# Kernel tuning notes

Measured on AMD Instinct MI355X. Metric: run time of the kernel, lower is better.

The kernel has to match this reference:

```python
import jax, jax.numpy as jnp
import numpy as np

WEIGHT = 1e-7
SIGMA_RGB = 15.0
SCALE = 0.5


def _nearest_resize(x, oh, ow):
    # PyTorch F.interpolate mode='nearest': src_idx = floor(dst * in/out)
    n, c, h, w = x.shape
    yi = (jnp.arange(oh) * (h / oh)).astype(jnp.int32)
    xi = (jnp.arange(ow) * (w / ow)).astype(jnp.int32)
    return x[:, :, yi][:, :, :, xi]


def _bilinear_resize(x, oh, ow):
    # PyTorch bilinear, align_corners=False: src = max((i+0.5)*in/out - 0.5, 0)
    n, k, h, w = x.shape

    def idx(o, s):
        src = jnp.maximum((jnp.arange(o, dtype=jnp.float32) + 0.5) * (s / o) - 0.5, 0.0)
        lo = jnp.floor(src).astype(jnp.int32)
        hi = jnp.minimum(lo + 1, s - 1)
        return lo, hi, src - lo

    ylo, yhi, fy = idx(oh, h)
    xlo, xhi, fx = idx(ow, w)
    top = x[:, :, ylo][:, :, :, xlo] * (1.0 - fx) + x[:, :, ylo][:, :, :, xhi] * fx
    bot = x[:, :, yhi][:, :, :, xlo] * (1.0 - fx) + x[:, :, yhi][:, :, :, xhi] * fx
    return top * (1.0 - fy)[:, None] + bot * fy[:, None]


def _bilateral_AS(feat, seg):
    # feat: [P,3] color features / sigma_rgb; seg: [K,P]
    # exact Gaussian color bilateral filter (what the permutohedral lattice approximates)
    sq = jnp.sum(feat * feat, axis=-1)                      # [P]
    d2 = sq[:, None] + sq[None, :] - 2.0 * (feat @ feat.T)  # [P,P]
    Kmat = jnp.exp(-0.5 * jnp.maximum(d2, 0.0))             # [P,P], symmetric
    return seg @ Kmat                                        # [K,P]


def setup_inputs() -> dict:
    key = jax.random.key(0)
    k1, k2 = jax.random.split(key)
    images = jax.random.uniform(k1, (4, 3, 128, 128), dtype=jnp.float32) * 255.0
    logits = jax.random.normal(k2, (4, 21, 128, 128), dtype=jnp.float32)
    segmentations = jax.nn.softmax(logits, axis=1)
    return {"images": images, "segmentations": segmentations}


def reference(images, segmentations):
    n, c, h, w = images.shape
    oh, ow = int(h * SCALE), int(w * SCALE)
    simg = _nearest_resize(images, oh, ow)            # [N,3,oh,ow]
    sseg = _bilinear_resize(segmentations, oh, ow)    # [N,K,oh,ow]
    P = oh * ow
    feats = simg.reshape(n, c, P).transpose(0, 2, 1) / SIGMA_RGB  # [N,P,3]
    segs = sseg.reshape(n, sseg.shape[1], P)                      # [N,K,P]
    AS = jax.vmap(_bilateral_AS)(feats, segs)                     # [N,K,P]
    loss = -jnp.sum(segs * AS) / jnp.float32(n)
    return (WEIGHT * loss).reshape(1)
```

## Files before the change

### kernel.cpp

```cpp
#include <hip/hip_runtime.h>


#define N_BATCH 4
#define IH 128
#define IW 128
#define P 4096
#define KC 21

using short8  = __attribute__((ext_vector_type(8))) short;
using floatx4 = __attribute__((ext_vector_type(4))) float;

static constexpr float INV_SIGMA = 1.0f / 15.0f;
static constexpr float LOG2E     = 1.4426950408889634f;
static constexpr float OUT_SCALE = -1e-7f / 4.0f;

#define ZP_OFF   0
#define ARGA_OFF 64
#define ARGB_OFF (ARGA_OFF + N_BATCH * P * 32)
#define SEG_OFF  (ARGB_OFF + N_BATCH * P * 32)

#define NFEAT (N_BATCH * P)
#define NSEG2 (N_BATCH * KC * P / 2)

__device__ __forceinline__ ushort f2bf(float x) {
    unsigned u = __builtin_bit_cast(unsigned, x);
    unsigned r = (u + 0x7FFFu + ((u >> 16) & 1u)) >> 16;
    return (ushort)r;
}
__device__ __forceinline__ float bf2f(ushort h) {
    return __builtin_bit_cast(float, (unsigned)h << 16);
}

__global__ void crf_prep(const float* __restrict__ img,
                         const float* __restrict__ seg,
                         char* __restrict__ wsb,
                         float* __restrict__ out)
{
    int t = blockIdx.x * blockDim.x + threadIdx.x;
    if (t < NFEAT) {
        if (t == 0) out[0] = 0.0f;
        if (t < 16) ((float*)(wsb + ZP_OFF))[t] = 0.0f;

        int n = t >> 12;
        int p = t & (P - 1);
        int y = p >> 6, x = p & 63;

        const float* ib = img + (size_t)n * 3 * IH * IW + (size_t)(2 * y) * IW + 2 * x;
        float f0 = ib[0] * INV_SIGMA;
        float f1 = ib[IH * IW] * INV_SIGMA;
        float f2 = ib[2 * IH * IW] * INV_SIGMA;
        float h = 0.5f * (f0 * f0 + f1 * f1 + f2 * f2);

        float fa0 = f0 * LOG2E, fa1 = f1 * LOG2E, fa2 = f2 * LOG2E;
        ushort ah0 = f2bf(fa0), ah1 = f2bf(fa1), ah2 = f2bf(fa2);
        ushort al0 = f2bf(fa0 - bf2f(ah0));
        ushort al1 = f2bf(fa1 - bf2f(ah1));
        ushort al2 = f2bf(fa2 - bf2f(ah2));
        float nhL = -h * LOG2E;
        ushort nhh = f2bf(nhL), nhl = f2bf(nhL - bf2f(nhh));
        ushort bh0 = f2bf(f0), bh1 = f2bf(f1), bh2 = f2bf(f2);
        ushort bl0 = f2bf(f0 - bf2f(bh0));
        ushort bl1 = f2bf(f1 - bf2f(bh1));
        ushort bl2 = f2bf(f2 - bf2f(bh2));
        float hL = h * LOG2E;
        ushort hbh = f2bf(hL), hbl = f2bf(hL - bf2f(hbh));

        const ushort ONE = 0x3F80, NEG1 = 0xBF80;
        ushort rA[16] = {ah0, ah1, ah2, ah0, ah1, ah2, al0, al1, al2, al0, al1, al2,
                         nhh, nhl, NEG1, NEG1};
        ushort rB[16] = {bh0, bh1, bh2, bl0, bl1, bl2, bh0, bh1, bh2, bl0, bl1, bl2,
                         ONE, ONE, hbh, hbl};

        short8 vA0, vA1, vB0, vB1;
#pragma unroll
        for (int j = 0; j < 8; ++j) {
            vA0[j] = (short)rA[j];     vA1[j] = (short)rA[8 + j];
            vB0[j] = (short)rB[j];     vB1[j] = (short)rB[8 + j];
        }
        short8* dA = (short8*)(wsb + ARGA_OFF + (size_t)t * 32);
        dA[0] = vA0; dA[1] = vA1;
        short8* dB = (short8*)(wsb + ARGB_OFF + (size_t)t * 32);
        dB[0] = vB0; dB[1] = vB1;

        char* sp = wsb + SEG_OFF + (size_t)t * 48;
        *(ushort*)(sp + 42) = 0;
        *(uint*)(sp + 44) = 0;
    } else if (t < NFEAT + NSEG2) {
        int u = t - NFEAT;
        int pp = (u & 2047) * 2;
        int nk = u >> 11;
        int n = nk / 21;
        int k = nk - n * 21;
        int y = pp >> 6, x0 = pp & 63;

        const float* r0 = seg + (size_t)nk * IH * IW + (size_t)(2 * y) * IW + 2 * x0;
        float4 a = *(const float4*)r0;
        float4 b = *(const float4*)(r0 + IW);
        float v0 = 0.25f * ((a.x + a.y) + (b.x + b.y));
        float v1 = 0.25f * ((a.z + a.w) + (b.z + b.w));
        char* d = wsb + SEG_OFF + (size_t)(n * P + pp) * 48 + k * 2;
        *(ushort*)d = f2bf(v0);
        *(ushort*)(d + 48) = f2bf(v1);
    }
}

__global__ __launch_bounds__(256, 4) void crf_pair(const char* __restrict__ wsb,
                                                   float* __restrict__ out)
{
    int n = blockIdx.z;
    int bp = blockIdx.y;
    int wave = threadIdx.x >> 6;
    int lane = threadIdx.x & 63;
    int quad = lane >> 4;
    int l16  = lane & 15;
    int w    = blockIdx.x * 4 + wave;

    const char* argA = wsb + ARGA_OFF + (size_t)n * P * 32;
    const char* argB = wsb + ARGB_OFF + (size_t)n * P * 32;
    const char* segT = wsb + SEG_OFF  + (size_t)n * P * 48;
    const char* zp   = wsb + ZP_OFF;

    int maskA = (quad < 2) ? ~0 : 0;
    int maskS = (quad < 3) ? ~0 : 0;
    const char* baseA_arg = (quad < 2) ? argA + quad * 16 : zp;
    const char* baseB_arg = (quad < 2) ? argB + quad * 16 : zp;
    const char* base_seg  = (quad < 3) ? segT + quad * 16 : zp;
    const int dA = 16384 & maskA;
    const int dS = 24576 & maskS;

    int s0 = 4 * bp;
    int s1 = 4 * (63 - bp);

    short8 aA0[4], aS0[4], aA1[4], aS1[4];
#pragma unroll
    for (int ii = 0; ii < 4; ++ii) {
        int r0 = (s0 + ii) * 16 + l16;
        int r1 = (s1 + ii) * 16 + l16;
        aA0[ii] = *(const short8*)(baseA_arg + ((r0 << 5) & maskA));
        aS0[ii] = *(const short8*)(base_seg  + ((r0 * 48) & maskS));
        aA1[ii] = *(const short8*)(baseA_arg + ((r1 << 5) & maskA));
        aS1[ii] = *(const short8*)(base_seg  + ((r1 * 48) & maskS));
    }

    float acc2 = 0.0f;
    float accE = 0.0f;
    floatx4 zero = {0.0f, 0.0f, 0.0f, 0.0f};

    {
        int cnt = 252 - s0;
        if (w < cnt) {
            int j = s0 + 4 + w;
            int r = (j << 4) + l16;
            int offA = (r << 5) & maskA;
            int offS = (r * 48) & maskS;
            int iters = ((cnt - w) + 31) >> 5;
            short8 b0a = *(const short8*)(baseB_arg + offA);
            short8 b0s = *(const short8*)(base_seg + offS);
            short8 b1a = b0a, b1s = b0s;
            if (iters > 1) {
                offA += dA; offS += dS;
                b1a = *(const short8*)(baseB_arg + offA);
                b1s = *(const short8*)(base_seg + offS);
            }
            for (int it = 0; it < iters; ++it) {
                short8 b2a = b0a, b2s = b0s;
                if (it + 2 < iters) {
                    offA += dA; offS += dS;
                    b2a = *(const short8*)(baseB_arg + offA);
                    b2s = *(const short8*)(base_seg + offS);
                }
#pragma unroll
                for (int ii = 0; ii < 4; ++ii) {
                    floatx4 g  = __builtin_amdgcn_mfma_f32_16x16x32_bf16(aS0[ii], b0s, zero, 0, 0, 0);
                    floatx4 ar = __builtin_amdgcn_mfma_f32_16x16x32_bf16(aA0[ii], b0a, zero, 0, 0, 0);
#pragma unroll
                    for (int jj = 0; jj < 4; ++jj)
                        acc2 += __builtin_amdgcn_exp2f(ar[jj]) * g[jj];
                }
                b0a = b1a; b0s = b1s; b1a = b2a; b1s = b2s;
            }
        }
    }

    {
        int cnt = 4 * bp;
        if (w < cnt) {
            int j = s1 + 4 + w;
            int r = (j << 4) + l16;
            int offA = (r << 5) & maskA;
            int offS = (r * 48) & maskS;
            int iters = ((cnt - w) + 31) >> 5;
            short8 b0a = *(const short8*)(baseB_arg + offA);
            short8 b0s = *(const short8*)(base_seg + offS);
            short8 b1a = b0a, b1s = b0s;
            if (iters > 1) {
                offA += dA; offS += dS;
                b1a = *(const short8*)(baseB_arg + offA);
                b1s = *(const short8*)(base_seg + offS);
            }
            for (int it = 0; it < iters; ++it) {
                short8 b2a = b0a, b2s = b0s;
                if (it + 2 < iters) {
                    offA += dA; offS += dS;
                    b2a = *(const short8*)(baseB_arg + offA);
                    b2s = *(const short8*)(base_seg + offS);
                }
#pragma unroll
                for (int ii = 0; ii < 4; ++ii) {
                    floatx4 g  = __builtin_amdgcn_mfma_f32_16x16x32_bf16(aS1[ii], b0s, zero, 0, 0, 0);
                    floatx4 ar = __builtin_amdgcn_mfma_f32_16x16x32_bf16(aA1[ii], b0a, zero, 0, 0, 0);
#pragma unroll
                    for (int jj = 0; jj < 4; ++jj)
                        acc2 += __builtin_amdgcn_exp2f(ar[jj]) * g[jj];
                }
                b0a = b1a; b0s = b1s; b1a = b2a; b1s = b2s;
            }
        }
    }

    if (w < 4) {
        int jrel = w;
        int r = ((s0 + jrel) << 4) + l16;
        short8 bArg = *(const short8*)(baseB_arg + ((r << 5) & maskA));
        short8 bSeg = *(const short8*)(base_seg  + ((r * 48) & maskS));
#pragma unroll
        for (int ii = 0; ii < 4; ++ii) {
            floatx4 g  = __builtin_amdgcn_mfma_f32_16x16x32_bf16(aS0[ii], bSeg, zero, 0, 0, 0);
            floatx4 ar = __builtin_amdgcn_mfma_f32_16x16x32_bf16(aA0[ii], bArg, zero, 0, 0, 0);
            float t = 0.0f;
#pragma unroll
            for (int jj = 0; jj < 4; ++jj)
                t += __builtin_amdgcn_exp2f(ar[jj]) * g[jj];
            float wt = (ii < jrel) ? 2.0f : ((ii == jrel) ? 1.0f : 0.0f);
            accE += wt * t;
        }
    }

    if (w >= 4 && w < 8) {
        int jrel = w - 4;
        int r = ((s1 + jrel) << 4) + l16;
        short8 bArg = *(const short8*)(baseB_arg + ((r << 5) & maskA));
        short8 bSeg = *(const short8*)(base_seg  + ((r * 48) & maskS));
#pragma unroll
        for (int ii = 0; ii < 4; ++ii) {
            floatx4 g  = __builtin_amdgcn_mfma_f32_16x16x32_bf16(aS1[ii], bSeg, zero, 0, 0, 0);
            floatx4 ar = __builtin_amdgcn_mfma_f32_16x16x32_bf16(aA1[ii], bArg, zero, 0, 0, 0);
            float t = 0.0f;
#pragma unroll
            for (int jj = 0; jj < 4; ++jj)
                t += __builtin_amdgcn_exp2f(ar[jj]) * g[jj];
            float wt = (ii < jrel) ? 2.0f : ((ii == jrel) ? 1.0f : 0.0f);
            accE += wt * t;
        }
    }

    float part = 2.0f * acc2 + accE;
#pragma unroll
    for (int off = 32; off > 0; off >>= 1)
        part += __shfl_down(part, off, 64);
    __shared__ float wsum[4];
    if (lane == 0) wsum[wave] = part;
    __syncthreads();
    if (threadIdx.x == 0)
        atomicAdd(out, ((wsum[0] + wsum[1]) + (wsum[2] + wsum[3])) * OUT_SCALE);
}

extern "C" void kernel_launch(void* const* d_in, const int* in_sizes, int n_in,
                              void* d_out, int out_size, void* d_ws, size_t ws_size,
                              hipStream_t stream)
{
    const float* images = (const float*)d_in[0];
    const float* segm   = (const float*)d_in[1];
    float* out = (float*)d_out;
    char* wsb = (char*)d_ws;

    int prep_threads = NFEAT + NSEG2;
    crf_prep<<<dim3((prep_threads + 255) / 256), dim3(256), 0, stream>>>(
        images, segm, wsb, out);
    crf_pair<<<dim3(8, 32, N_BATCH), dim3(256), 0, stream>>>(wsb, out);
}
```

Measured before the change: 78.90 us.

## Switch pairwise kernel to 32x32x16 MFMA tiles with new chunked work split

Replaces the 16x16x32 bf16 MFMA tiling with 32x32x16 tiles. Each wave now owns one 32-row A tile and sweeps B tiles in strided chunks across 16 blocks in x. The upper-triangle work split is redone for 32-row tiles, with diagonal blocks handled by designated chunk blocks. The goal is fewer MFMA issues per output element and better operand reuse. The cost is a third MFMA to cover the 21-class K dimension (split across two k-slices) and more accumulator registers.

```diff
diff --git a/kernel.cpp b/kernel.cpp
--- a/kernel.cpp
+++ b/kernel.cpp
@@ -7,8 +7,8 @@
 #define P 4096
 #define KC 21
 
-using short8  = __attribute__((ext_vector_type(8))) short;
-using floatx4 = __attribute__((ext_vector_type(4))) float;
+using short8   = __attribute__((ext_vector_type(8))) short;
+using floatx16 = __attribute__((ext_vector_type(16))) float;
 
 static constexpr float INV_SIGMA = 1.0f / 15.0f;
 static constexpr float LOG2E     = 1.4426950408889634f;
@@ -21,6 +21,8 @@
 
 #define NFEAT (N_BATCH * P)
 #define NSEG2 (N_BATCH * KC * P / 2)
+
+#define CHUNKS 16
 
 __device__ __forceinline__ ushort f2bf(float x) {
     unsigned u = __builtin_bit_cast(unsigned, x);
@@ -107,154 +109,124 @@
 __global__ __launch_bounds__(256, 4) void crf_pair(const char* __restrict__ wsb,
                                                    float* __restrict__ out)
 {
-    int n = blockIdx.z;
-    int bp = blockIdx.y;
-    int wave = threadIdx.x >> 6;
-    int lane = threadIdx.x & 63;
-    int quad = lane >> 4;
-    int l16  = lane & 15;
-    int w    = blockIdx.x * 4 + wave;
+    const int n    = blockIdx.z;
+    const int sp   = blockIdx.y;
+    const int c    = blockIdx.x;
+    const int wave = threadIdx.x >> 6;
+    const int lane = threadIdx.x & 63;
+    const int l32  = lane & 31;
+    const int l5   = lane >> 5;
 
     const char* argA = wsb + ARGA_OFF + (size_t)n * P * 32;
     const char* argB = wsb + ARGB_OFF + (size_t)n * P * 32;
     const char* segT = wsb + SEG_OFF  + (size_t)n * P * 48;
     const char* zp   = wsb + ZP_OFF;
 
-    int maskA = (quad < 2) ? ~0 : 0;
-    int maskS = (quad < 3) ? ~0 : 0;
-    const char* baseA_arg = (quad < 2) ? argA + quad * 16 : zp;
-    const char* baseB_arg = (quad < 2) ? argB + quad * 16 : zp;
-    const char* base_seg  = (quad < 3) ? segT + quad * 16 : zp;
-    const int dA = 16384 & maskA;
-    const int dS = 24576 & maskS;
-
-    int s0 = 4 * bp;
-    int s1 = 4 * (63 - bp);
-
-    short8 aA0[4], aS0[4], aA1[4], aS1[4];
-#pragma unroll
-    for (int ii = 0; ii < 4; ++ii) {
-        int r0 = (s0 + ii) * 16 + l16;
-        int r1 = (s1 + ii) * 16 + l16;
-        aA0[ii] = *(const short8*)(baseA_arg + ((r0 << 5) & maskA));
-        aS0[ii] = *(const short8*)(base_seg  + ((r0 * 48) & maskS));
-        aA1[ii] = *(const short8*)(baseA_arg + ((r1 << 5) & maskA));
-        aS1[ii] = *(const short8*)(base_seg  + ((r1 * 48) & maskS));
-    }
-
-    float acc2 = 0.0f;
-    float accE = 0.0f;
-    floatx4 zero = {0.0f, 0.0f, 0.0f, 0.0f};
-
-    {
-        int cnt = 252 - s0;
-        if (w < cnt) {
-            int j = s0 + 4 + w;
-            int r = (j << 4) + l16;
-            int offA = (r << 5) & maskA;
-            int offS = (r * 48) & maskS;
-            int iters = ((cnt - w) + 31) >> 5;
-            short8 b0a = *(const short8*)(baseB_arg + offA);
-            short8 b0s = *(const short8*)(base_seg + offS);
-            short8 b1a = b0a, b1s = b0s;
-            if (iters > 1) {
-                offA += dA; offS += dS;
-                b1a = *(const short8*)(baseB_arg + offA);
-                b1s = *(const short8*)(base_seg + offS);
+    const char* bBa = argB + l32 * 32 + l5 * 16;
+    const char* bBs = segT + l32 * 48 + l5 * 16;
+    const int maskH = l5 ? 0 : ~0;
+    const char* bBh = l5 ? zp : (segT + l32 * 48 + 32);
+
+    const floatx16 zc = {0.f,0.f,0.f,0.f,0.f,0.f,0.f,0.f,
+                         0.f,0.f,0.f,0.f,0.f,0.f,0.f,0.f};
+
+    short8 afA, afL, afH;
+
+    float m0=0.f, m1=0.f, m2=0.f, m3=0.f;
+    float d0=0.f, d1=0.f, d2=0.f, d3=0.f;
+
+    auto jobM = [&](short8 ba, short8 bl, short8 bh) {
+        floatx16 ar = __builtin_amdgcn_mfma_f32_32x32x16_bf16(afA, ba, zc, 0, 0, 0);
+        floatx16 g  = __builtin_amdgcn_mfma_f32_32x32x16_bf16(afL, bl, zc, 0, 0, 0);
+        g = __builtin_amdgcn_mfma_f32_32x32x16_bf16(afH, bh, g, 0, 0, 0);
+#pragma unroll
+        for (int r = 0; r < 16; ++r) {
+            float t = __builtin_amdgcn_exp2f(ar[r]) * g[r];
+            if ((r & 3) == 0) m0 += t;
+            else if ((r & 3) == 1) m1 += t;
+            else if ((r & 3) == 2) m2 += t;
+            else m3 += t;
+        }
+    };
+    auto jobD = [&](short8 ba, short8 bl, short8 bh) {
+        floatx16 ar = __builtin_amdgcn_mfma_f32_32x32x16_bf16(afA, ba, zc, 0, 0, 0);
+        floatx16 g  = __builtin_amdgcn_mfma_f32_32x32x16_bf16(afL, bl, zc, 0, 0, 0);
+        g = __builtin_amdgcn_mfma_f32_32x32x16_bf16(afH, bh, g, 0, 0, 0);
+#pragma unroll
+        for (int r = 0; r < 16; ++r) {
+            float t = __builtin_amdgcn_exp2f(ar[r]) * g[r];
+            if ((r & 3) == 0) d0 += t;
+            else if ((r & 3) == 1) d1 += t;
+            else if ((r & 3) == 2) d2 += t;
+            else d3 += t;
+        }
+    };
+
+    auto load_A = [&](int ti) {
+        int rr = ti * 32 + l32;
+        afA = *(const short8*)(argA + rr * 32 + l5 * 16);
+        afL = *(const short8*)(segT + rr * 48 + l5 * 16);
+        afH = l5 ? *(const short8*)zp : *(const short8*)(segT + rr * 48 + 32);
+    };
+
+    auto run_main = [&](int jbase, int cnt) {
+        if (cnt <= c) return;
+        int nj = (cnt - c + CHUNKS - 1) / CHUNKS;
+        int j0 = jbase + c;
+        int oA0 = j0 * 1024, oS0 = j0 * 1536;
+        int oA1 = oA0 + CHUNKS * 1024, oS1 = oS0 + CHUNKS * 1536;
+        short8 a0 = *(const short8*)(bBa + oA0);
+        short8 l0 = *(const short8*)(bBs + oS0);
+        short8 h0 = *(const short8*)(bBh + (oS0 & maskH));
+        short8 a1 = a0, l1 = l0, h1 = h0;
+        if (nj > 1) {
+            a1 = *(const short8*)(bBa + oA1);
+            l1 = *(const short8*)(bBs + oS1);
+            h1 = *(const short8*)(bBh + (oS1 & maskH));
+        }
+        for (int t = 0; t < nj; t += 2) {
+            jobM(a0, l0, h0);
+            if (t + 2 < nj) {
+                oA0 += 2 * CHUNKS * 1024; oS0 += 2 * CHUNKS * 1536;
+                a0 = *(const short8*)(bBa + oA0);
+                l0 = *(const short8*)(bBs + oS0);
+                h0 = *(const short8*)(bBh + (oS0 & maskH));
             }
-            for (int it = 0; it < iters; ++it) {
-                short8 b2a = b0a, b2s = b0s;
-                if (it + 2 < iters) {
-                    offA += dA; offS += dS;
-                    b2a = *(const short8*)(baseB_arg + offA);
-                    b2s = *(const short8*)(base_seg + offS);
+            if (t + 1 < nj) {
+                jobM(a1, l1, h1);
+                if (t + 3 < nj) {
+                    oA1 += 2 * CHUNKS * 1024; oS1 += 2 * CHUNKS * 1536;
+                    a1 = *(const short8*)(bBa + oA1);
+                    l1 = *(const short8*)(bBs + oS1);
+                    h1 = *(const short8*)(bBh + (oS1 & maskH));
                 }
-#pragma unroll
-                for (int ii = 0; ii < 4; ++ii) {
-                    floatx4 g  = __builtin_amdgcn_mfma_f32_16x16x32_bf16(aS0[ii], b0s, zero, 0, 0, 0);
-                    floatx4 ar = __builtin_amdgcn_mfma_f32_16x16x32_bf16(aA0[ii], b0a, zero, 0, 0, 0);
-#pragma unroll
-                    for (int jj = 0; jj < 4; ++jj)
-                        acc2 += __builtin_amdgcn_exp2f(ar[jj]) * g[jj];
-                }
-                b0a = b1a; b0s = b1s; b1a = b2a; b1s = b2s;
             }
         }
-    }
-
-    {
-        int cnt = 4 * bp;
-        if (w < cnt) {
-            int j = s1 + 4 + w;
-            int r = (j << 4) + l16;
-            int offA = (r << 5) & maskA;
-            int offS = (r * 48) & maskS;
-            int iters = ((cnt - w) + 31) >> 5;
-            short8 b0a = *(const short8*)(baseB_arg + offA);
-            short8 b0s = *(const short8*)(base_seg + offS);
-            short8 b1a = b0a, b1s = b0s;
-            if (iters > 1) {
-                offA += dA; offS += dS;
-                b1a = *(const short8*)(baseB_arg + offA);
-                b1s = *(const short8*)(base_seg + offS);
-            }
-            for (int it = 0; it < iters; ++it) {
-                short8 b2a = b0a, b2s = b0s;
-                if (it + 2 < iters) {
-                    offA += dA; offS += dS;
-                    b2a = *(const short8*)(baseB_arg + offA);
-                    b2s = *(const short8*)(base_seg + offS);
-                }
-#pragma unroll
-                for (int ii = 0; ii < 4; ++ii) {
-                    floatx4 g  = __builtin_amdgcn_mfma_f32_16x16x32_bf16(aS1[ii], b0s, zero, 0, 0, 0);
-                    floatx4 ar = __builtin_amdgcn_mfma_f32_16x16x32_bf16(aA1[ii], b0a, zero, 0, 0, 0);
-#pragma unroll
-                    for (int jj = 0; jj < 4; ++jj)
-                        acc2 += __builtin_amdgcn_exp2f(ar[jj]) * g[jj];
-                }
-                b0a = b1a; b0s = b1s; b1a = b2a; b1s = b2s;
-            }
-        }
-    }
-
-    if (w < 4) {
-        int jrel = w;
-        int r = ((s0 + jrel) << 4) + l16;
-        short8 bArg = *(const short8*)(baseB_arg + ((r << 5) & maskA));
-        short8 bSeg = *(const short8*)(base_seg  + ((r * 48) & maskS));
-#pragma unroll
-        for (int ii = 0; ii < 4; ++ii) {
-            floatx4 g  = __builtin_amdgcn_mfma_f32_16x16x32_bf16(aS0[ii], bSeg, zero, 0, 0, 0);
-            floatx4 ar = __builtin_amdgcn_mfma_f32_16x16x32_bf16(aA0[ii], bArg, zero, 0, 0, 0);
-            float t = 0.0f;
-#pragma unroll
-            for (int jj = 0; jj < 4; ++jj)
-                t += __builtin_amdgcn_exp2f(ar[jj]) * g[jj];
-            float wt = (ii < jrel) ? 2.0f : ((ii == jrel) ? 1.0f : 0.0f);
-            accE += wt * t;
-        }
-    }
-
-    if (w >= 4 && w < 8) {
-        int jrel = w - 4;
-        int r = ((s1 + jrel) << 4) + l16;
-        short8 bArg = *(const short8*)(baseB_arg + ((r << 5) & maskA));
-        short8 bSeg = *(const short8*)(base_seg  + ((r * 48) & maskS));
-#pragma unroll
-        for (int ii = 0; ii < 4; ++ii) {
-            floatx4 g  = __builtin_amdgcn_mfma_f32_16x16x32_bf16(aS1[ii], bSeg, zero, 0, 0, 0);
-            floatx4 ar = __builtin_amdgcn_mfma_f32_16x16x32_bf16(aA1[ii], bArg, zero, 0, 0, 0);
-            float t = 0.0f;
-#pragma unroll
-            for (int jj = 0; jj < 4; ++jj)
-                t += __builtin_amdgcn_exp2f(ar[jj]) * g[jj];
-            float wt = (ii < jrel) ? 2.0f : ((ii == jrel) ? 1.0f : 0.0f);
-            accE += wt * t;
-        }
-    }
-
-    float part = 2.0f * acc2 + accE;
+    };
+
+    auto run_edge = [&](int s) {
+        for (int jj = wave; jj < 4; ++jj) {
+            int j = 4 * s + jj;
+            int oA = j * 1024, oS = j * 1536;
+            short8 ba = *(const short8*)(bBa + oA);
+            short8 bl = *(const short8*)(bBs + oS);
+            short8 bh = *(const short8*)(bBh + (oS & maskH));
+            if (jj == wave) jobD(ba, bl, bh);
+            else           jobM(ba, bl, bh);
+        }
+    };
+
+    const int s0 = sp, s1 = 31 - sp;
+
+    load_A(4 * s0 + wave);
+    run_main(4 * s0 + 4, 124 - 4 * sp);
+    if (c == CHUNKS - 1) run_edge(s0);
+
+    load_A(4 * s1 + wave);
+    run_main(4 * s1 + 4, 4 * sp);
+    if (c == CHUNKS - 2) run_edge(s1);
+
+    float part = 2.0f * ((m0 + m1) + (m2 + m3)) + ((d0 + d1) + (d2 + d3));
 #pragma unroll
     for (int off = 32; off > 0; off >>= 1)
         part += __shfl_down(part, off, 64);
@@ -277,5 +249,5 @@
     int prep_threads = NFEAT + NSEG2;
     crf_prep<<<dim3((prep_threads + 255) / 256), dim3(256), 0, stream>>>(
         images, segm, wsb, out);
-    crf_pair<<<dim3(8, 32, N_BATCH), dim3(256), 0, stream>>>(wsb, out);
-}
+    crf_pair<<<dim3(CHUNKS, 16, N_BATCH), dim3(256), 0, stream>>>(wsb, out);
+}
```

Result: no change. 78.75 us (-0.2%).
